# Kernel tuning notes

Measured on AMD Instinct MI355X. Metric: run time of the kernel, lower is better.

The kernel has to match this reference:

```python
import jax, jax.numpy as jnp
import numpy as np

L, S, N, E, H = 1024, 1024, 4, 1024, 16


def setup_inputs() -> dict:
    key = jax.random.key(0)
    ks = jax.random.split(key, 7)
    return {
        "query": jax.random.normal(ks[0], (L, N, E), jnp.float32),
        "key": jax.random.normal(ks[1], (S, N, E), jnp.float32),
        "value": jax.random.normal(ks[2], (S, N, E), jnp.float32),
        "in_proj_weight": jax.random.normal(ks[3], (3 * E, E), jnp.float32) * (E ** -0.5),
        "in_proj_bias": jax.random.normal(ks[4], (3 * E,), jnp.float32) * 0.02,
        "out_proj_weight": jax.random.normal(ks[5], (E, E), jnp.float32) * (E ** -0.5),
        "out_proj_bias": jax.random.normal(ks[6], (E,), jnp.float32) * 0.02,
        "num_heads": H,
    }


def _split_heads(x, n, h, hd):
    # (T, N, E) -> (N*h, T, hd), matching torch view(T, N*h, hd).transpose(0, 1)
    t = x.shape[0]
    return jnp.transpose(x.reshape(t, n * h, hd), (1, 0, 2))


def reference(query, key, value, in_proj_weight, in_proj_bias,
              out_proj_weight, out_proj_bias, num_heads):
    tgt_len, bsz, embed_dim = query.shape
    src_len = key.shape[0]
    head_dim = embed_dim // num_heads
    scaling = float(head_dim) ** -0.5

    # packed QKV projection (torch F.linear: x @ W.T + b), sliced as in source
    q = query @ in_proj_weight[:embed_dim].T + in_proj_bias[:embed_dim]
    k = key @ in_proj_weight[embed_dim:2 * embed_dim].T + in_proj_bias[embed_dim:2 * embed_dim]
    v = value @ in_proj_weight[2 * embed_dim:].T + in_proj_bias[2 * embed_dim:]
    q = q * scaling

    q = _split_heads(q, bsz, num_heads, head_dim)  # (N*H, L, hd)
    k = _split_heads(k, bsz, num_heads, head_dim)  # (N*H, S, hd)
    v = _split_heads(v, bsz, num_heads, head_dim)  # (N*H, S, hd)

    scores = jnp.einsum('bld,bsd->bls', q, k)           # (N*H, L, S)
    attn = jax.nn.softmax(scores, axis=-1)
    ctx = jnp.einsum('bls,bsd->bld', attn, v)           # (N*H, L, hd)

    # (N*H, L, hd) -> (L, N, E)
    ctx = jnp.transpose(ctx, (1, 0, 2)).reshape(tgt_len, bsz, embed_dim)
    attn_output = ctx @ out_proj_weight.T + out_proj_bias

    # need_weights=True path: average over heads -> (N, L, S)
    attn_weights = attn.reshape(bsz, num_heads, tgt_len, src_len).sum(axis=1) / num_heads
    return attn_output, attn_weights
```

## Files before the change

### kernel.cpp

```cpp
#include <hip/hip_runtime.h>

typedef unsigned short u16;
typedef __attribute__((ext_vector_type(8))) short short8;
typedef __attribute__((ext_vector_type(4))) float f32x4;

__device__ __forceinline__ u16 f2bf(float f) {
  unsigned int i = __float_as_uint(f);
  i += 0x7fffu + ((i >> 16) & 1u);
  return (u16)(i >> 16);
}

__device__ __forceinline__ short8 cvt8(const float* p) {
  float4 a = ((const float4*)p)[0];
  float4 b = ((const float4*)p)[1];
  short8 r;
  r[0] = (short)f2bf(a.x); r[1] = (short)f2bf(a.y);
  r[2] = (short)f2bf(a.z); r[3] = (short)f2bf(a.w);
  r[4] = (short)f2bf(b.x); r[5] = (short)f2bf(b.y);
  r[6] = (short)f2bf(b.z); r[7] = (short)f2bf(b.w);
  return r;
}

__global__ __launch_bounds__(256) void convert_bf16(
    const float* __restrict__ q, const float* __restrict__ k,
    const float* __restrict__ v, const float* __restrict__ Wi,
    const float* __restrict__ Wo,
    u16* __restrict__ qb, u16* __restrict__ kb, u16* __restrict__ vb,
    u16* __restrict__ Wib, u16* __restrict__ Wob)
{
  const float* src; u16* dst; int len8;
  switch (blockIdx.y) {
    case 0:  src = q;  dst = qb;  len8 = 524288; break;
    case 1:  src = k;  dst = kb;  len8 = 524288; break;
    case 2:  src = v;  dst = vb;  len8 = 524288; break;
    case 3:  src = Wi; dst = Wib; len8 = 393216; break;
    default: src = Wo; dst = Wob; len8 = 131072; break;
  }
  int stride = gridDim.x * 256;
  for (int i = blockIdx.x * 256 + threadIdx.x; i < len8; i += stride)
    *(short8*)(dst + (size_t)i * 8) = cvt8(src + (size_t)i * 8);
}

__global__ __launch_bounds__(256) void qkv_gemm(
    const u16* __restrict__ qb, const u16* __restrict__ kb,
    const u16* __restrict__ vb, const u16* __restrict__ W,
    const float* __restrict__ bias,
    u16* __restrict__ qh, u16* __restrict__ kh, u16* __restrict__ vt)
{
  __shared__ __align__(16) u16 SH[24576];

  const int tid  = threadIdx.x;
  const int wave = tid >> 6;
  const int lane = tid & 63;
  const int r    = lane & 15;
  const int q4   = lane >> 4;
  const int wm   = wave >> 1;
  const int wn   = wave & 1;

  const int orig = blockIdx.y * 24 + blockIdx.x;
  const int nid  = (orig & 7) * 96 + (orig >> 3);
  const int mt   = nid / 24;
  const int jt   = nid - mt * 24;
  const int src  = jt >> 3;
  const u16* X = (src == 0) ? qb : (src == 1) ? kb : vb;
  const int m0 = mt * 128;
  const int j0 = jt * 128;

  const int lrow = lane >> 2;
  const int lchk = ((lane & 3) ^ ((lane >> 3) & 3)) << 4;
  const char* Xc = (const char*)X;
  const char* Wc = (const char*)W;
  const int fchk = (q4 ^ ((r >> 1) & 3)) << 3;

  f32x4 acc[4][4];
  #pragma unroll
  for (int a = 0; a < 4; ++a)
    #pragma unroll
    for (int b = 0; b < 4; ++b)
      acc[a][b] = (f32x4){0.f, 0.f, 0.f, 0.f};

  auto STAGE = [&](int buf, int kt) {
    const int kbyte = kt * 64;
    u16* Ad = SH + buf * 4096;
    u16* Bd = SH + 12288 + buf * 4096;
    #pragma unroll
    for (int i = 0; i < 2; ++i) {
      const int g = wave * 2 + i;
      __builtin_amdgcn_global_load_lds(
          (const u16*)(Xc + (size_t)(m0 + g * 16 + lrow) * 2048 + kbyte + lchk),
          Ad + g * 512, 16, 0, 0);
      __builtin_amdgcn_global_load_lds(
          (const u16*)(Wc + (size_t)(j0 + g * 16 + lrow) * 2048 + kbyte + lchk),
          Bd + g * 512, 16, 0, 0);
    }
  };

  auto COMPUTE = [&](int cb) {
    const u16* As = SH + cb * 4096;
    const u16* Bs = SH + 12288 + cb * 4096;
    short8 af[4], bf[4];
    #pragma unroll
    for (int mi = 0; mi < 4; ++mi)
      af[mi] = *(const short8*)(&As[(wm * 64 + mi * 16 + r) * 32 + fchk]);
    #pragma unroll
    for (int ji = 0; ji < 4; ++ji)
      bf[ji] = *(const short8*)(&Bs[(wn * 64 + ji * 16 + r) * 32 + fchk]);
    #pragma unroll
    for (int mi = 0; mi < 4; ++mi)
      #pragma unroll
      for (int ji = 0; ji < 4; ++ji)
        acc[mi][ji] = __builtin_amdgcn_mfma_f32_16x16x32_bf16(af[mi], bf[ji], acc[mi][ji], 0, 0, 0);
  };

  STAGE(0, 0);
  STAGE(1, 1);
  int cb = 0;
  for (int kt = 0; kt < 31; ++kt) {
    asm volatile("s_waitcnt vmcnt(4) lgkmcnt(0)\n\ts_barrier" ::: "memory");
    if (kt < 30) {
      int nb = cb + 2; if (nb >= 3) nb -= 3;
      STAGE(nb, kt + 2);
    }
    COMPUTE(cb);
    if (++cb == 3) cb = 0;
  }
  asm volatile("s_waitcnt vmcnt(0) lgkmcnt(0)\n\ts_barrier" ::: "memory");
  COMPUTE(cb);

  __syncthreads();
  const int h0 = (j0 & 1023) >> 6;
  const int t0 = mt * 32;
  if (src < 2) {
    #pragma unroll
    for (int mi = 0; mi < 4; ++mi) {
      const int tt = wm * 16 + mi * 4 + q4;
      #pragma unroll
      for (int ji = 0; ji < 4; ++ji) {
        const int jj = wn * 64 + ji * 16 + r;
        const int dd = jj & 63, hq = jj >> 6;
        const int cs = (((dd >> 3) ^ (tt & 7)) << 3) + (dd & 7);
        #pragma unroll
        for (int rr = 0; rr < 4; ++rr) {
          float v = acc[mi][ji][rr] + bias[j0 + jj];
          SH[((rr * 2 + hq) * 32 + tt) * 64 + cs] =
              (src == 0) ? f2bf(v * 0.125f) : f2bf(v);
        }
      }
    }
    __syncthreads();
    u16* dst = (src == 0) ? qh : kh;
    #pragma unroll
    for (int c = 0; c < 8; ++c) {
      const int cid = c * 256 + tid;
      const int nn = cid >> 9, hq = (cid >> 8) & 1, tt = (cid >> 3) & 31, dc = cid & 7;
      short8 vv = *(const short8*)(SH + ((nn * 2 + hq) * 32 + tt) * 64 +
                                   ((dc ^ (tt & 7)) << 3));
      *(short8*)(dst + (size_t)(nn * 16 + h0 + hq) * 65536 +
                 (size_t)(t0 + tt) * 64 + dc * 8) = vv;
    }
  } else {
    #pragma unroll
    for (int mi = 0; mi < 4; ++mi) {
      const int tt = wm * 16 + mi * 4 + q4;
      const int tc = tt >> 3, toff = tt & 7;
      #pragma unroll
      for (int ji = 0; ji < 4; ++ji) {
        const int jj = wn * 64 + ji * 16 + r;
        const int dd = jj & 63, hq = jj >> 6;
        #pragma unroll
        for (int rr = 0; rr < 4; ++rr) {
          float v = acc[mi][ji][rr] + bias[j0 + jj];
          SH[((rr * 2 + hq) * 64 + dd) * 32 + ((tc ^ (dd & 3)) << 3) + toff] = f2bf(v);
        }
      }
    }
    __syncthreads();
    #pragma unroll
    for (int c = 0; c < 8; ++c) {
      const int cid = c * 256 + tid;
      const int bbv = cid >> 8, dd = (cid >> 2) & 63, tc = cid & 3;
      short8 vv = *(const short8*)(SH + (bbv * 64 + dd) * 32 +
                                   ((tc ^ (dd & 3)) << 3));
      const int bb = (bbv >> 1) * 16 + h0 + (bbv & 1);
      *(short8*)(vt + (size_t)bb * 65536 + (size_t)dd * 1024 + t0 + tc * 8) = vv;
    }
  }
}

__global__ __launch_bounds__(256) void attn_ctx_mfma(
    const u16* __restrict__ qh, const u16* __restrict__ kh,
    const u16* __restrict__ vt, u16* __restrict__ ctx,
    float* __restrict__ Zbuf)
{
  __shared__ __align__(16) u16 Ks[2][4096];
  __shared__ __align__(16) u16 Vs[2][4096];
  __shared__ __align__(16) u16 Pl[4][1024];

  const int tid = threadIdx.x;
  const int wv = tid >> 6, lane = tid & 63, r = lane & 15, q4 = lane >> 4;
  const int b  = blockIdx.y;
  const int lw = blockIdx.x * 64 + wv * 16;
  const int n = b >> 4, h = b & 15;

  const u16* qbase = qh + (size_t)b * 65536;
  const char* kc = (const char*)(kh + (size_t)b * 65536);
  const char* vc = (const char*)(vt + (size_t)b * 65536);
  u16* P = Pl[wv];

  const int ls  = lane >> 3;
  const int swzb = ((lane & 7) ^ ls) << 4;
  const int iw  = wv * 2;
  const size_t klo = (size_t)iw * 1024 + (size_t)ls * 128 + swzb;
  const size_t vlo = (size_t)iw * 16384 + (size_t)ls * 2048 + swzb;

  const int rsw = r & 7;
  const int c0 = (q4 ^ rsw) << 3;
  const int c1 = ((q4 ^ rsw) ^ 4) << 3;

  short8 aq0 = *(const short8*)(qbase + (size_t)(lw + r) * 64 + q4 * 8);
  short8 aq1 = *(const short8*)(qbase + (size_t)(lw + r) * 64 + 32 + q4 * 8);

  f32x4 oc[4];
  #pragma unroll
  for (int ji = 0; ji < 4; ++ji) oc[ji] = (f32x4){0.f, 0.f, 0.f, 0.f};
  float z[4] = {0.f, 0.f, 0.f, 0.f};

  {
    const char* kp = kc + klo;
    const char* vp = vc + vlo;
    u16* kd = &Ks[0][iw * 512];
    u16* vd = &Vs[0][iw * 512];
    __builtin_amdgcn_global_load_lds(kp,          kd,       16, 0, 0);
    __builtin_amdgcn_global_load_lds(kp + 1024,   kd + 512, 16, 0, 0);
    __builtin_amdgcn_global_load_lds(vp,          vd,       16, 0, 0);
    __builtin_amdgcn_global_load_lds(vp + 16384,  vd + 512, 16, 0, 0);
  }

  for (int it = 0; it < 16; ++it) {
    const int cur = it & 1;
    __syncthreads();
    const u16* Kb = Ks[cur];
    const u16* Vb = Vs[cur];

    f32x4 sc[4];
    #pragma unroll
    for (int ji = 0; ji < 4; ++ji) {
      const int row = (ji * 16 + r) * 64;
      short8 bk0 = *(const short8*)(Kb + row + c0);
      short8 bk1 = *(const short8*)(Kb + row + c1);
      f32x4 t = (f32x4){0.f, 0.f, 0.f, 0.f};
      t = __builtin_amdgcn_mfma_f32_16x16x32_bf16(aq0, bk0, t, 0, 0, 0);
      t = __builtin_amdgcn_mfma_f32_16x16x32_bf16(aq1, bk1, t, 0, 0, 0);
      sc[ji] = t;
    }

    if (it < 15) {
      const char* kp = kc + (size_t)(it + 1) * 8192 + klo;
      const char* vp = vc + (size_t)(it + 1) * 128  + vlo;
      u16* kd = &Ks[cur ^ 1][iw * 512];
      u16* vd = &Vs[cur ^ 1][iw * 512];
      __builtin_amdgcn_global_load_lds(kp,          kd,       16, 0, 0);
      __builtin_amdgcn_global_load_lds(kp + 1024,   kd + 512, 16, 0, 0);
      __builtin_amdgcn_global_load_lds(vp,          vd,       16, 0, 0);
      __builtin_amdgcn_global_load_lds(vp + 16384,  vd + 512, 16, 0, 0);
    }

    #pragma unroll
    for (int ji = 0; ji < 4; ++ji) {
      const int cw = ji * 2 + (r >> 3);
      #pragma unroll
      for (int rr = 0; rr < 4; ++rr) {
        float e = __expf(sc[ji][rr]);
        z[rr] += e;
        const int row = q4 * 4 + rr;
        P[row * 64 + ((cw ^ (row & 7)) << 3) + (r & 7)] = f2bf(e);
      }
    }
    asm volatile("s_waitcnt lgkmcnt(0)" ::: "memory");
    short8 ap0 = *(const short8*)(P + r * 64 + c0);
    short8 ap1 = *(const short8*)(P + r * 64 + c1);
    #pragma unroll
    for (int ji = 0; ji < 4; ++ji) {
      const int row = (ji * 16 + r) * 64;
      short8 bv0 = *(const short8*)(Vb + row + c0);
      short8 bv1 = *(const short8*)(Vb + row + c1);
      oc[ji] = __builtin_amdgcn_mfma_f32_16x16x32_bf16(ap0, bv0, oc[ji], 0, 0, 0);
      oc[ji] = __builtin_amdgcn_mfma_f32_16x16x32_bf16(ap1, bv1, oc[ji], 0, 0, 0);
    }
  }

  #pragma unroll
  for (int rr = 0; rr < 4; ++rr) {
    float zz = z[rr];
    zz += __shfl_xor(zz, 1);
    zz += __shfl_xor(zz, 2);
    zz += __shfl_xor(zz, 4);
    zz += __shfl_xor(zz, 8);
    z[rr] = zz;
  }

  #pragma unroll
  for (int rr = 0; rr < 4; ++rr) {
    float inv = 1.0f / z[rr];
    int l = lw + q4 * 4 + rr;
    u16* crow = ctx + ((size_t)l * 4 + n) * 1024 + h * 64;
    #pragma unroll
    for (int ji = 0; ji < 4; ++ji)
      crow[ji * 16 + r] = f2bf(oc[ji][rr] * inv);
    if (r == 0) Zbuf[(size_t)b * 1024 + l] = z[rr];
  }
}

__global__ __launch_bounds__(256) void tail_fused(
    const u16* __restrict__ qh, const u16* __restrict__ kh,
    const float* __restrict__ Zbuf, float* __restrict__ out_w,
    const u16* __restrict__ ctx, const u16* __restrict__ W,
    const float* __restrict__ bias, float* __restrict__ out)
{
  __shared__ __align__(16) u16 SH[18432];

  const int tid = threadIdx.x;
  const int wv = tid >> 6, lane = tid & 63, r = lane & 15, q4 = lane >> 4;

  if (blockIdx.x < 512) {
    const int wave = wv;
    const int wm   = wave >> 1;
    const int wn   = wave & 1;
    const int orig = blockIdx.x;
    const int nid  = (orig & 7) * 64 + (orig >> 3);
    const int mt   = nid >> 4;
    const int jt   = nid & 15;
    const int m0 = mt * 128;
    const int j0 = jt * 64;

    const int lrow = lane >> 2;
    const int lchk = ((lane & 3) ^ ((lane >> 3) & 3)) << 4;
    const char* Ac = (const char*)ctx;
    const char* Wc = (const char*)W;
    const int fchk = (q4 ^ ((r >> 1) & 3)) << 3;

    f32x4 acc[4][2];
    #pragma unroll
    for (int a = 0; a < 4; ++a)
      #pragma unroll
      for (int b = 0; b < 2; ++b)
        acc[a][b] = (f32x4){0.f, 0.f, 0.f, 0.f};

    auto STAGE = [&](int buf, int kt) {
      const int kbyte = kt * 64;
      u16* Ad = SH + buf * 4096;
      u16* Bd = SH + 12288 + buf * 2048;
      #pragma unroll
      for (int i = 0; i < 2; ++i) {
        const int g = wave * 2 + i;
        __builtin_amdgcn_global_load_lds(
            (const u16*)(Ac + (size_t)(m0 + g * 16 + lrow) * 2048 + kbyte + lchk),
            Ad + g * 512, 16, 0, 0);
      }
      __builtin_amdgcn_global_load_lds(
          (const u16*)(Wc + (size_t)(j0 + wave * 16 + lrow) * 2048 + kbyte + lchk),
          Bd + wave * 512, 16, 0, 0);
    };

    auto COMPUTE = [&](int cb) {
      const u16* As = SH + cb * 4096;
      const u16* Bs = SH + 12288 + cb * 2048;
      short8 af[4], bf[2];
      #pragma unroll
      for (int mi = 0; mi < 4; ++mi)
        af[mi] = *(const short8*)(&As[(wm * 64 + mi * 16 + r) * 32 + fchk]);
      #pragma unroll
      for (int ji = 0; ji < 2; ++ji)
        bf[ji] = *(const short8*)(&Bs[(wn * 32 + ji * 16 + r) * 32 + fchk]);
      #pragma unroll
      for (int mi = 0; mi < 4; ++mi)
        #pragma unroll
        for (int ji = 0; ji < 2; ++ji)
          acc[mi][ji] = __builtin_amdgcn_mfma_f32_16x16x32_bf16(af[mi], bf[ji], acc[mi][ji], 0, 0, 0);
    };

    STAGE(0, 0);
    STAGE(1, 1);
    int cb = 0;
    for (int kt = 0; kt < 31; ++kt) {
      asm volatile("s_waitcnt vmcnt(3) lgkmcnt(0)\n\ts_barrier" ::: "memory");
      if (kt < 30) {
        int nb = cb + 2; if (nb >= 3) nb -= 3;
        STAGE(nb, kt + 2);
      }
      COMPUTE(cb);
      if (++cb == 3) cb = 0;
    }
    asm volatile("s_waitcnt vmcnt(0) lgkmcnt(0)\n\ts_barrier" ::: "memory");
    COMPUTE(cb);

    #pragma unroll
    for (int mi = 0; mi < 4; ++mi) {
      #pragma unroll
      for (int ji = 0; ji < 2; ++ji) {
        #pragma unroll
        for (int rr = 0; rr < 4; ++rr) {
          int m = m0 + wm * 64 + mi * 16 + q4 * 4 + rr;
          int j = j0 + wn * 32 + ji * 16 + r;
          out[(size_t)m * 1024 + j] = acc[mi][ji][rr] + bias[j];
        }
      }
    }
  } else {
    const int id2 = blockIdx.x - 512;
    const int lt = id2 & 15;
    const int st = (id2 >> 4) & 15;
    const int n  = id2 >> 8;
    const int l0 = lt * 64;
    const int s0 = st * 64;
    const int lw = l0 + wv * 16;

    u16* Kw = SH;
    float* invZ = (float*)(SH + 8192);

    const char* khc = (const char*)kh + (size_t)n * 2097152;

    const int ls  = lane >> 3;
    const int swzb = ((lane & 7) ^ ls) << 4;
    const int iw  = wv * 2;
    const size_t klo = (size_t)s0 * 128 + (size_t)iw * 1024 + (size_t)ls * 128 + swzb;

    const int rsw = r & 7;
    const int c0 = (q4 ^ rsw) << 3;
    const int c1 = ((q4 ^ rsw) ^ 4) << 3;

    for (int i = tid; i < 1024; i += 256) {
      int hh = i >> 6, row = i & 63;
      invZ[hh * 64 + row] = 1.0f / (Zbuf[(size_t)(n * 16 + hh) * 1024 + l0 + row] * 16.0f);
    }

    {
      const char* kp = khc + klo;
      u16* kd = &Kw[iw * 512];
      __builtin_amdgcn_global_load_lds(kp,        kd,       16, 0, 0);
      __builtin_amdgcn_global_load_lds(kp + 1024, kd + 512, 16, 0, 0);
    }
    const u16* q0 = qh + (size_t)(n * 16) * 65536;
    short8 aqc0 = *(const short8*)(q0 + (size_t)(lw + r) * 64 + q4 * 8);
    short8 aqc1 = *(const short8*)(q0 + (size_t)(lw + r) * 64 + 32 + q4 * 8);

    f32x4 wacc[4];
    #pragma unroll
    for (int ji = 0; ji < 4; ++ji) wacc[ji] = (f32x4){0.f, 0.f, 0.f, 0.f};

    for (int hh = 0; hh < 16; ++hh) {
      const int cur = hh & 1;
      __syncthreads();
      if (hh < 15) {
        const char* kp = khc + (size_t)(hh + 1) * 131072 + klo;
        u16* kd = &Kw[(cur ^ 1) * 4096 + iw * 512];
        __builtin_amdgcn_global_load_lds(kp,        kd,       16, 0, 0);
        __builtin_amdgcn_global_load_lds(kp + 1024, kd + 512, 16, 0, 0);
      }
      const int hn = (hh < 15) ? hh + 1 : hh;
      const u16* qn = qh + (size_t)(n * 16 + hn) * 65536;
      short8 an0 = *(const short8*)(qn + (size_t)(lw + r) * 64 + q4 * 8);
      short8 an1 = *(const short8*)(qn + (size_t)(lw + r) * 64 + 32 + q4 * 8);

      const u16* Kb = Kw + cur * 4096;
      f32x4 sc[4];
      #pragma unroll
      for (int ji = 0; ji < 4; ++ji) {
        const int row = (ji * 16 + r) * 64;
        short8 bk0 = *(const short8*)(Kb + row + c0);
        short8 bk1 = *(const short8*)(Kb + row + c1);
        f32x4 t = (f32x4){0.f, 0.f, 0.f, 0.f};
        t = __builtin_amdgcn_mfma_f32_16x16x32_bf16(aqc0, bk0, t, 0, 0, 0);
        t = __builtin_amdgcn_mfma_f32_16x16x32_bf16(aqc1, bk1, t, 0, 0, 0);
        sc[ji] = t;
      }
      #pragma unroll
      for (int rr = 0; rr < 4; ++rr) {
        float iv = invZ[hh * 64 + wv * 16 + q4 * 4 + rr];
        #pragma unroll
        for (int ji = 0; ji < 4; ++ji)
          wacc[ji][rr] += __expf(sc[ji][rr]) * iv;
      }
      aqc0 = an0; aqc1 = an1;
    }

    #pragma unroll
    for (int ji = 0; ji < 4; ++ji)
      #pragma unroll
      for (int rr = 0; rr < 4; ++rr) {
        int row = lw + q4 * 4 + rr;
        int col = s0 + ji * 16 + r;
        out_w[(size_t)n * 1048576 + (size_t)row * 1024 + col] = wacc[ji][rr];
      }
  }
}

extern "C" void kernel_launch(void* const* d_in, const int* in_sizes, int n_in,
                              void* d_out, int out_size, void* d_ws, size_t ws_size,
                              hipStream_t stream) {
  const float* query = (const float*)d_in[0];
  const float* key   = (const float*)d_in[1];
  const float* value = (const float*)d_in[2];
  const float* W_in  = (const float*)d_in[3];
  const float* b_in  = (const float*)d_in[4];
  const float* W_out = (const float*)d_in[5];
  const float* b_out = (const float*)d_in[6];
  float* out = (float*)d_out;

  u16* qb  = (u16*)d_ws;
  u16* kb  = qb  + (size_t)4194304;
  u16* vb  = kb  + (size_t)4194304;
  u16* Wib = vb  + (size_t)4194304;
  u16* Wob = Wib + (size_t)3145728;
  u16* qh  = Wob + (size_t)1048576;
  u16* kh  = qh  + (size_t)4194304;
  u16* vt  = kh  + (size_t)4194304;
  u16* ctx = vt  + (size_t)4194304;
  float* Zbuf = (float*)(ctx + (size_t)4194304);

  convert_bf16<<<dim3(512, 5), 256, 0, stream>>>(query, key, value, W_in, W_out,
                                                 qb, kb, vb, Wib, Wob);
  qkv_gemm<<<dim3(24, 32), 256, 0, stream>>>(qb, kb, vb, Wib, b_in, qh, kh, vt);
  attn_ctx_mfma<<<dim3(16, 64), 256, 0, stream>>>(qh, kh, vt, ctx, Zbuf);
  tail_fused<<<dim3(1536), 256, 0, stream>>>(qh, kh, Zbuf, out + (size_t)4194304,
                                             ctx, Wob, b_out, out);
}
```

Before: 224.6 us.

## Triple-buffer K tiles in LDS with partial vmcnt waits in weights branch

The attention-weights branch now keeps three LDS buffers for per-head K tiles instead of two, prefetching two heads ahead. Each iteration ends its wait with an explicit `s_waitcnt vmcnt(4)` plus a barrier instead of `__syncthreads`, so the newest prefetches can stay in flight while the current head is computed. The goal is to hide global-to-LDS load latency across the 16-head loop. In exchange it uses more LDS, which may lower occupancy, and it depends on hand-counted vmcnt ordering being correct.

```diff
diff --git a/kernel.cpp b/kernel.cpp
--- a/kernel.cpp
+++ b/kernel.cpp
@@ -416,7 +416,7 @@
     const int lw = l0 + wv * 16;
 
     u16* Kw = SH;
-    float* invZ = (float*)(SH + 8192);
+    float* invZ = (float*)(SH + 12288);
 
     const char* khc = (const char*)kh + (size_t)n * 2097152;
 
@@ -434,12 +434,15 @@
       invZ[hh * 64 + row] = 1.0f / (Zbuf[(size_t)(n * 16 + hh) * 1024 + l0 + row] * 16.0f);
     }
 
-    {
-      const char* kp = khc + klo;
-      u16* kd = &Kw[iw * 512];
+    auto STAGEK = [&](int buf, int hh) {
+      const char* kp = khc + (size_t)hh * 131072 + klo;
+      u16* kd = &Kw[buf * 4096 + iw * 512];
       __builtin_amdgcn_global_load_lds(kp,        kd,       16, 0, 0);
       __builtin_amdgcn_global_load_lds(kp + 1024, kd + 512, 16, 0, 0);
-    }
+    };
+
+    STAGEK(0, 0);
+    STAGEK(1, 1);
     const u16* q0 = qh + (size_t)(n * 16) * 65536;
     short8 aqc0 = *(const short8*)(q0 + (size_t)(lw + r) * 64 + q4 * 8);
     short8 aqc1 = *(const short8*)(q0 + (size_t)(lw + r) * 64 + 32 + q4 * 8);
@@ -448,21 +451,16 @@
     #pragma unroll
     for (int ji = 0; ji < 4; ++ji) wacc[ji] = (f32x4){0.f, 0.f, 0.f, 0.f};
 
-    for (int hh = 0; hh < 16; ++hh) {
-      const int cur = hh & 1;
-      __syncthreads();
-      if (hh < 15) {
-        const char* kp = khc + (size_t)(hh + 1) * 131072 + klo;
-        u16* kd = &Kw[(cur ^ 1) * 4096 + iw * 512];
-        __builtin_amdgcn_global_load_lds(kp,        kd,       16, 0, 0);
-        __builtin_amdgcn_global_load_lds(kp + 1024, kd + 512, 16, 0, 0);
-      }
+    auto HEAD = [&](int hh, int cbw, short8& an0, short8& an1) {
       const int hn = (hh < 15) ? hh + 1 : hh;
       const u16* qn = qh + (size_t)(n * 16 + hn) * 65536;
-      short8 an0 = *(const short8*)(qn + (size_t)(lw + r) * 64 + q4 * 8);
-      short8 an1 = *(const short8*)(qn + (size_t)(lw + r) * 64 + 32 + q4 * 8);
-
-      const u16* Kb = Kw + cur * 4096;
+      an0 = *(const short8*)(qn + (size_t)(lw + r) * 64 + q4 * 8);
+      an1 = *(const short8*)(qn + (size_t)(lw + r) * 64 + 32 + q4 * 8);
+      if (hh < 14) {
+        int nb = cbw + 2; if (nb >= 3) nb -= 3;
+        STAGEK(nb, hh + 2);
+      }
+      const u16* Kb = Kw + cbw * 4096;
       f32x4 sc[4];
       #pragma unroll
       for (int ji = 0; ji < 4; ++ji) {
@@ -482,7 +480,17 @@
           wacc[ji][rr] += __expf(sc[ji][rr]) * iv;
       }
       aqc0 = an0; aqc1 = an1;
-    }
+    };
+
+    int cbw = 0;
+    short8 an0, an1;
+    for (int hh = 0; hh < 15; ++hh) {
+      asm volatile("s_waitcnt vmcnt(4) lgkmcnt(0)\n\ts_barrier" ::: "memory");
+      HEAD(hh, cbw, an0, an1);
+      if (++cbw == 3) cbw = 0;
+    }
+    asm volatile("s_waitcnt vmcnt(0) lgkmcnt(0)\n\ts_barrier" ::: "memory");
+    HEAD(15, cbw, an0, an1);
 
     #pragma unroll
     for (int ji = 0; ji < 4; ++ji)
```

Measured after the change: 223.3 us. Within noise of the previous version (-0.6%).
